# Performance work log

Measured on AMD Instinct MI355X. Metric: run time of the kernel, lower is better.

## Reference

```python
import jax, jax.numpy as jnp
import numpy as np

B, S, HID = 2, 1024, 2048
H, HK, D = 32, 4, 128
G = H // HK
EPS = 1e-6
SCALE = 1.0 / np.sqrt(D)
ROPE_THETA = 1000000.0


def _rope_tables(seq_len, dim, theta):
    inv_freq = 1.0 / (theta ** (np.arange(0, dim, 2, dtype=np.float32) / dim))
    t = np.arange(seq_len, dtype=np.float32)
    freqs = np.outer(t, inv_freq)                      # [S, D/2]
    emb = np.concatenate([freqs, freqs], axis=-1)       # [S, D]
    return (jnp.asarray(np.cos(emb))[None, :, None, :],
            jnp.asarray(np.sin(emb))[None, :, None, :])  # [1,S,1,D]


def setup_inputs() -> dict:
    key = jax.random.key(0)
    k1, k2, k3 = jax.random.split(key, 3)
    cos, sin = _rope_tables(S, D, ROPE_THETA)
    return {
        "hidden_states": jax.random.normal(k1, (B, S, HID), jnp.float32),
        "cos": cos,
        "sin": sin,
        "w_qkv": jax.random.normal(k2, (HID, (H + 2 * HK) * D), jnp.float32) * 0.02,
        "q_norm_w": jnp.ones((D,), jnp.float32),
        "k_norm_w": jnp.ones((D,), jnp.float32),
        "w_o": jax.random.normal(k3, (H * D, HID), jnp.float32) * 0.02,
    }


def _rms_norm(x, w):
    xf = x.astype(jnp.float32)
    var = jnp.mean(xf * xf, axis=-1, keepdims=True)
    return (w * (xf * jax.lax.rsqrt(var + EPS))).astype(x.dtype)


def _rotate_half(x):
    x1, x2 = jnp.split(x, 2, axis=-1)
    return jnp.concatenate([-x2, x1], axis=-1)


def reference(hidden_states, cos, sin, w_qkv, q_norm_w, k_norm_w, w_o):
    b, s, _ = hidden_states.shape
    qkv = hidden_states @ w_qkv                          # [B,S,(H+2HK)*D]
    q, k, v = jnp.split(qkv, [H * D, (H + HK) * D], axis=-1)
    q = q.reshape(b, s, H, D)
    k = k.reshape(b, s, HK, D)
    v = v.reshape(b, s, HK, D)
    # per-head RMSNorm on q/k, then rotary (BSH layout)
    q = _rms_norm(q, q_norm_w)
    k = _rms_norm(k, k_norm_w)
    q = q * cos + _rotate_half(q) * sin
    k = k * cos + _rotate_half(k) * sin
    # grouped-query causal SDPA (prefill path, sparse_mode=2)
    qg = q.reshape(b, s, HK, G, D)
    scores = jnp.einsum("bqkgd,bskd->bkgqs", qg, k) * SCALE  # [B,HK,G,S,S]
    causal = jnp.tril(jnp.ones((s, s), bool))
    scores = jnp.where(causal, scores, jnp.finfo(scores.dtype).min)
    probs = jax.nn.softmax(scores, axis=-1)
    ctx = jnp.einsum("bkgqs,bskd->bqkgd", probs, v)          # [B,S,HK,G,D]
    ctx = ctx.reshape(b, s, H * D)
    return ctx @ w_o                                          # [B,S,HID]
```

## Files before the change

### kernel.cpp

```cpp
#include <hip/hip_runtime.h>

#define B_   2
#define S_   1024
#define HID_ 2048
#define H_   32
#define HK_  4
#define D_   128
#define NQKV ((H_ + 2 * HK_) * D_)
#define TOK  (B_ * S_)

typedef short bf16x8  __attribute__((ext_vector_type(8)));
typedef short short4v __attribute__((ext_vector_type(4)));
typedef float f32x4   __attribute__((ext_vector_type(4)));
typedef int   i32x4   __attribute__((ext_vector_type(4)));

__device__ inline short f2bf(float f) {
  unsigned u = __builtin_bit_cast(unsigned, f);
  u += 0x7fffu + ((u >> 16) & 1u);
  return (short)(u >> 16);
}
__device__ inline float bf2f(short s) {
  return __builtin_bit_cast(float, ((unsigned)(unsigned short)s) << 16);
}

__device__ __forceinline__ void gld_lds16(const short* g, short* l) {
  __builtin_amdgcn_global_load_lds((__attribute__((address_space(1))) void*)g,
                                   (__attribute__((address_space(3))) void*)l, 16, 0, 0);
}

__global__ __launch_bounds__(256) void cast_f32_bf16(const float* __restrict__ in,
                                                     short* __restrict__ out, int n4) {
  int i = blockIdx.x * 256 + threadIdx.x;
  if (i >= n4) return;
  f32x4 v = ((const f32x4*)in)[i];
  short4v o;
  o[0] = f2bf(v[0]); o[1] = f2bf(v[1]); o[2] = f2bf(v[2]); o[3] = f2bf(v[3]);
  ((short4v*)out)[i] = o;
}

__global__ __launch_bounds__(256) void transpose_cast(const float* __restrict__ in,
                                                      short* __restrict__ out,
                                                      int K, int N) {
  __shared__ float tile[32][33];
  int nb = blockIdx.x * 32, kb = blockIdx.y * 32;
  int c = threadIdx.x & 31, r0 = threadIdx.x >> 5;
#pragma unroll
  for (int i = 0; i < 4; i++) {
    int r = r0 + i * 8;
    tile[r][c] = in[(size_t)(kb + r) * N + nb + c];
  }
  __syncthreads();
#pragma unroll
  for (int i = 0; i < 4; i++) {
    int r = r0 + i * 8;
    out[(size_t)(nb + r) * K + kb + c] = f2bf(tile[c][r]);
  }
}

__global__ __launch_bounds__(256) void gemm_bt128(const short* __restrict__ A,
                                                  const short* __restrict__ Bt,
                                                  float* __restrict__ C,
                                                  int M, int N, int Kfull, int klen) {
  const int tid  = threadIdx.x;
  const int m0   = blockIdx.y * 128;
  const int n0   = blockIdx.x * 128;
  const int kz0  = blockIdx.z * klen;
  const int w    = tid >> 6, lane = tid & 63;
  const int quad = lane >> 4, l16 = lane & 15;
  const int wm   = (w >> 1) * 64, wn = (w & 1) * 64;

  __shared__ short As[128 * 64];
  __shared__ short Bs[128 * 64];

  const f32x4 z = {0.f, 0.f, 0.f, 0.f};
  f32x4 acc[4][4];
#pragma unroll
  for (int i = 0; i < 4; i++)
#pragma unroll
    for (int j = 0; j < 4; j++) acc[i][j] = z;

  const int srow = lane >> 3;
  const int lc   = (lane & 7) ^ srow;

  for (int kk = 0; kk < klen; kk += 64) {
    const int k0 = kz0 + kk;
#pragma unroll
    for (int i = 0; i < 4; i++) {
      int rb = w * 32 + i * 8;
      gld_lds16(&A [(size_t)(m0 + rb + srow) * Kfull + k0 + lc * 8], &As[rb * 64]);
      gld_lds16(&Bt[(size_t)(n0 + rb + srow) * Kfull + k0 + lc * 8], &Bs[rb * 64]);
    }
    __syncthreads();
#pragma unroll
    for (int kb = 0; kb < 2; kb++) {
      const int pc = ((kb * 4 + quad) ^ (l16 & 7)) * 8;
      bf16x8 a[4], b[4];
#pragma unroll
      for (int f = 0; f < 4; f++) {
        a[f] = *(const bf16x8*)&As[(wm + f * 16 + l16) * 64 + pc];
        b[f] = *(const bf16x8*)&Bs[(wn + f * 16 + l16) * 64 + pc];
      }
#pragma unroll
      for (int fi = 0; fi < 4; fi++)
#pragma unroll
        for (int fj = 0; fj < 4; fj++)
          acc[fi][fj] = __builtin_amdgcn_mfma_f32_16x16x32_bf16(a[fi], b[fj], acc[fi][fj], 0, 0, 0);
    }
    __syncthreads();
  }

  float* Cz = C + (size_t)blockIdx.z * M * N;
#pragma unroll
  for (int fi = 0; fi < 4; fi++) {
    int row0 = m0 + wm + fi * 16 + quad * 4;
#pragma unroll
    for (int fj = 0; fj < 4; fj++) {
      int col = n0 + wn + fj * 16 + l16;
#pragma unroll
      for (int r = 0; r < 4; r++)
        Cz[(size_t)(row0 + r) * N + col] = acc[fi][fj][r];
    }
  }
}

__global__ __launch_bounds__(256) void add2(const float* __restrict__ a,
                                            const float* __restrict__ b,
                                            float* __restrict__ c, int n4) {
  int i = blockIdx.x * 256 + threadIdx.x;
  if (i >= n4) return;
  f32x4 va = ((const f32x4*)a)[i], vb = ((const f32x4*)b)[i];
  ((f32x4*)c)[i] = va + vb;
}

__global__ __launch_bounds__(256) void gemm_qkv(const short* __restrict__ A,
                                                const short* __restrict__ Bt,
                                                const float* __restrict__ cosT,
                                                const float* __restrict__ sinT,
                                                const float* __restrict__ qw,
                                                const float* __restrict__ kw,
                                                short* __restrict__ Qb,
                                                short* __restrict__ Kb,
                                                short* __restrict__ Vt) {
  const int tid  = threadIdx.x;
  const int m0   = blockIdx.y * 128;
  const int n0   = blockIdx.x * 128;
  const int w    = tid >> 6, lane = tid & 63;
  const int quad = lane >> 4, l16 = lane & 15;
  const int wm   = (w >> 1) * 64, wn = (w & 1) * 64;

  __shared__ short As[128 * 64];
  __shared__ short Bs[128 * 64];
  __shared__ float ss_lds[4][64];

  const f32x4 z = {0.f, 0.f, 0.f, 0.f};
  f32x4 acc[4][4];
#pragma unroll
  for (int i = 0; i < 4; i++)
#pragma unroll
    for (int j = 0; j < 4; j++) acc[i][j] = z;

  const int srow = lane >> 3;
  const int lc   = (lane & 7) ^ srow;

  for (int k0 = 0; k0 < HID_; k0 += 64) {
#pragma unroll
    for (int i = 0; i < 4; i++) {
      int rb = w * 32 + i * 8;
      gld_lds16(&A [(size_t)(m0 + rb + srow) * HID_ + k0 + lc * 8], &As[rb * 64]);
      gld_lds16(&Bt[(size_t)(n0 + rb + srow) * HID_ + k0 + lc * 8], &Bs[rb * 64]);
    }
    __syncthreads();
#pragma unroll
    for (int kb = 0; kb < 2; kb++) {
      const int pc = ((kb * 4 + quad) ^ (l16 & 7)) * 8;
      bf16x8 a[4], b[4];
#pragma unroll
      for (int f = 0; f < 4; f++) {
        a[f] = *(const bf16x8*)&As[(wm + f * 16 + l16) * 64 + pc];
        b[f] = *(const bf16x8*)&Bs[(wn + f * 16 + l16) * 64 + pc];
      }
#pragma unroll
      for (int fi = 0; fi < 4; fi++)
#pragma unroll
        for (int fj = 0; fj < 4; fj++)
          acc[fi][fj] = __builtin_amdgcn_mfma_f32_16x16x32_bf16(a[fi], b[fj], acc[fi][fj], 0, 0, 0);
    }
    __syncthreads();
  }

  const int hd = n0 >> 7;
  const int bb = m0 >> 10;
  const int sW = (m0 & (S_ - 1)) + wm;

  if (hd >= H_ + HK_) {
    const int khv = hd - (H_ + HK_);
    short* dstV = Vt + ((size_t)(bb * HK_ + khv) * D_) * S_;
#pragma unroll
    for (int fi = 0; fi < 4; fi++) {
      int s = sW + fi * 16 + quad * 4;
#pragma unroll
      for (int fj = 0; fj < 4; fj++) {
        int d = wn + fj * 16 + l16;
        short4v o;
#pragma unroll
        for (int r = 0; r < 4; r++) o[r] = f2bf(acc[fi][fj][r]);
        *(short4v*)&dstV[(size_t)d * S_ + s] = o;
      }
    }
    return;
  }

  float ssp[4][4];
#pragma unroll
  for (int fi = 0; fi < 4; fi++)
#pragma unroll
    for (int r = 0; r < 4; r++) {
      float t = 0.f;
#pragma unroll
      for (int fj = 0; fj < 4; fj++) t += acc[fi][fj][r] * acc[fi][fj][r];
      ssp[fi][r] = t;
    }
#pragma unroll
  for (int off = 1; off < 16; off <<= 1)
#pragma unroll
    for (int fi = 0; fi < 4; fi++)
#pragma unroll
      for (int r = 0; r < 4; r++) ssp[fi][r] += __shfl_xor(ssp[fi][r], off, 64);
  if (l16 == 0)
#pragma unroll
    for (int fi = 0; fi < 4; fi++)
#pragma unroll
      for (int r = 0; r < 4; r++) ss_lds[w][fi * 16 + quad * 4 + r] = ssp[fi][r];
  __syncthreads();
  float rn[4][4];
#pragma unroll
  for (int fi = 0; fi < 4; fi++)
#pragma unroll
    for (int r = 0; r < 4; r++) {
      int row = fi * 16 + quad * 4 + r;
      rn[fi][r] = rsqrtf((ss_lds[w][row] + ss_lds[w ^ 1][row]) * (1.0f / 128.0f) + 1e-6f);
    }
  const float* wv = (hd < H_) ? qw : kw;
  float wgt[4];
#pragma unroll
  for (int fj = 0; fj < 4; fj++) wgt[fj] = wv[wn + fj * 16 + l16];

  short* xown = (w & 1) ? &Bs[(w >> 1) * 4096] : &As[(w >> 1) * 4096];
  short* xpar = (w & 1) ? &As[(w >> 1) * 4096] : &Bs[(w >> 1) * 4096];
#pragma unroll
  for (int fi = 0; fi < 4; fi++)
#pragma unroll
    for (int fj = 0; fj < 4; fj++) {
      short4v y4;
#pragma unroll
      for (int r = 0; r < 4; r++) y4[r] = f2bf(acc[fi][fj][r] * rn[fi][r] * wgt[fj]);
      *(short4v*)&xown[(((fi * 4 + fj) * 4 + quad) * 16 + l16) * 4] = y4;
    }
  __syncthreads();

  const float sign = (wn == 0) ? -1.0f : 1.0f;
  const float osc  = (hd < H_) ? (0.08838834764831845f * 1.4426950408889634f) : 1.0f;
  short* dstQ = (hd < H_) ? (Qb + (((size_t)bb * H_ + hd) * S_) * D_)
                          : (Kb + (((size_t)bb * HK_ + (hd - H_)) * S_) * D_);
#pragma unroll
  for (int fi = 0; fi < 4; fi++)
#pragma unroll
    for (int fj = 0; fj < 4; fj++) {
      short4v yp4 = *(const short4v*)&xpar[(((fi * 4 + fj) * 4 + quad) * 16 + l16) * 4];
      int d = wn + fj * 16 + l16;
#pragma unroll
      for (int r = 0; r < 4; r++) {
        int s = sW + fi * 16 + quad * 4 + r;
        float y  = acc[fi][fj][r] * rn[fi][r] * wgt[fj];
        float yp = bf2f(yp4[r]);
        float c  = cosT[s * D_ + d];
        float sn = sinT[s * D_ + d];
        dstQ[(size_t)s * D_ + d] = f2bf((y * c + sign * yp * sn) * osc);
      }
    }
}

__global__ __launch_bounds__(256) void attn_mfma5(const short* __restrict__ Qb,
                                                  const short* __restrict__ Kb,
                                                  const short* __restrict__ Vt,
                                                  short* __restrict__ ctx) {
  const int qmap[8] = {7, 0, 6, 1, 5, 2, 4, 3};
  const int qt = qmap[blockIdx.x & 7];
  const int h  = blockIdx.y;
  const int b  = blockIdx.z;
  const int kh = h >> 3;
  const int q0 = qt * 128;
  const int tid = threadIdx.x, w = tid >> 6, lane = tid & 63;
  const int quad = lane >> 4, l16 = lane & 15;
  const float MBIAS = 18.0f;

  __shared__ short Ks[128 * 64];
  __shared__ short Vs[144 * 64];
  __shared__ short Ps[4][2][16 * 72];

  for (int i = tid; i < 16 * 64; i += 256) Vs[128 * 64 + i] = (short)0x3F80;

  const short* Qbase = Qb + (((size_t)b * H_ + h) * S_ + q0) * D_;
  bf16x8 aq[2][4];
#pragma unroll
  for (int fi = 0; fi < 2; fi++)
#pragma unroll
    for (int kb = 0; kb < 4; kb++)
      aq[fi][kb] = *(const bf16x8*)&Qbase[(size_t)(fi * 64 + w * 16 + l16) * D_ + kb * 32 + quad * 8];

  const f32x4 z = {0.f, 0.f, 0.f, 0.f};
  f32x4 O[2][9];
#pragma unroll
  for (int fi = 0; fi < 2; fi++)
#pragma unroll
    for (int n = 0; n < 9; n++) O[fi][n] = z;

  const short* Kbase = Kb + ((size_t)(b * HK_ + kh) * S_) * D_;
  const short* Vbase = Vt + ((size_t)(b * HK_ + kh) * D_) * S_;

  const int srow = lane >> 3;
  const int lc   = (lane & 7) ^ srow;

  const int nkt = 2 * qt + 2;
  for (int kt = 0; kt < nkt; kt++) {
    const int k0 = kt * 64;
    __syncthreads();
#pragma unroll
    for (int i = 0; i < 4; i++) {
      int rb = w * 32 + i * 8;
      int rr = rb + srow;
      gld_lds16(&Kbase[(size_t)(k0 + (rr & 63)) * D_ + (rr >> 6) * 64 + lc * 8], &Ks[rb * 64]);
      gld_lds16(&Vbase[(size_t)rr * S_ + k0 + lc * 8], &Vs[rb * 64]);
    }
    __syncthreads();

#pragma unroll
    for (int nb = 0; nb < 4; nb++) {
      f32x4 s0 = z, s1 = z;
#pragma unroll
      for (int kb = 0; kb < 4; kb++) {
        const int c  = kb * 4 + quad;
        const int c7 = c & 7;
        const int rr = (c >> 3) * 64 + nb * 16 + l16;
        bf16x8 bk = *(const bf16x8*)&Ks[rr * 64 + (c7 ^ (l16 & 7)) * 8];
        s0 = __builtin_amdgcn_mfma_f32_16x16x32_bf16(aq[0][kb], bk, s0, 0, 0, 0);
        s1 = __builtin_amdgcn_mfma_f32_16x16x32_bf16(aq[1][kb], bk, s1, 0, 0, 0);
      }
      const int col = k0 + nb * 16 + l16;
#pragma unroll
      for (int r = 0; r < 4; r++) {
        int row0 = q0 + w * 16 + quad * 4 + r;
        float p0 = (col > row0) ? 0.0f : exp2f(s0[r] - MBIAS);
        float p1 = (col > row0 + 64) ? 0.0f : exp2f(s1[r] - MBIAS);
        Ps[w][0][(quad * 4 + r) * 72 + nb * 16 + l16] = f2bf(p0);
        Ps[w][1][(quad * 4 + r) * 72 + nb * 16 + l16] = f2bf(p1);
      }
    }

#pragma unroll
    for (int kb2 = 0; kb2 < 2; kb2++) {
      bf16x8 ap0 = *(const bf16x8*)&Ps[w][0][l16 * 72 + kb2 * 32 + quad * 8];
      bf16x8 ap1 = *(const bf16x8*)&Ps[w][1][l16 * 72 + kb2 * 32 + quad * 8];
      const int c7 = kb2 * 4 + quad;
#pragma unroll
      for (int nb2 = 0; nb2 < 9; nb2++) {
        int d = nb2 * 16 + l16;
        bf16x8 bv = *(const bf16x8*)&Vs[d * 64 + (c7 ^ (d & 7)) * 8];
        O[0][nb2] = __builtin_amdgcn_mfma_f32_16x16x32_bf16(ap0, bv, O[0][nb2], 0, 0, 0);
        O[1][nb2] = __builtin_amdgcn_mfma_f32_16x16x32_bf16(ap1, bv, O[1][nb2], 0, 0, 0);
      }
    }
  }

#pragma unroll
  for (int fi = 0; fi < 2; fi++)
#pragma unroll
    for (int r = 0; r < 4; r++) {
      float inv = 1.0f / O[fi][8][r];
      size_t row = (size_t)(b * S_ + q0 + fi * 64 + w * 16 + quad * 4 + r);
      short* dst = ctx + row * (H_ * D_) + h * D_;
#pragma unroll
      for (int nb2 = 0; nb2 < 8; nb2++)
        dst[nb2 * 16 + l16] = f2bf(O[fi][nb2][r] * inv);
    }
}

extern "C" void kernel_launch(void* const* d_in, const int* in_sizes, int n_in,
                              void* d_out, int out_size, void* d_ws, size_t ws_size,
                              hipStream_t stream) {
  (void)in_sizes; (void)n_in; (void)out_size; (void)ws_size;
  const float* hidden = (const float*)d_in[0];
  const float* cosT   = (const float*)d_in[1];
  const float* sinT   = (const float*)d_in[2];
  const float* wqkv   = (const float*)d_in[3];
  const float* qnw    = (const float*)d_in[4];
  const float* knw    = (const float*)d_in[5];
  const float* wo     = (const float*)d_in[6];
  float* out = (float*)d_out;

  char* ws = (char*)d_ws;
  short* Qb  = (short*)ws;
  short* Kb  = (short*)(ws + 16777216);
  short* Vt  = (short*)(ws + 16777216 + 2097152);
  short* hb  = (short*)(ws + 41943040);
  short* wT  = (short*)(ws + 41943040 + 8388608);
  short* ctx = (short*)(ws + 41943040 + 8388608 + 20971520);
  float* part = (float*)ws;

  cast_f32_bf16<<<4096, 256, 0, stream>>>(hidden, hb, TOK * HID_ / 4);
  transpose_cast<<<dim3(NQKV / 32, HID_ / 32), 256, 0, stream>>>(wqkv, wT, HID_, NQKV);
  gemm_qkv<<<dim3(NQKV / 128, TOK / 128), 256, 0, stream>>>(hb, wT, cosT, sinT, qnw, knw, Qb, Kb, Vt);
  attn_mfma5<<<dim3(S_ / 128, H_, B_), 256, 0, stream>>>(Qb, Kb, Vt, ctx);
  transpose_cast<<<dim3(HID_ / 32, (H_ * D_) / 32), 256, 0, stream>>>(wo, wT, H_ * D_, HID_);
  gemm_bt128<<<dim3(HID_ / 128, TOK / 128, 2), 256, 0, stream>>>(ctx, wT, part, TOK, HID_, H_ * D_, (H_ * D_) / 2);
  add2<<<(TOK * HID_ / 4 + 255) / 256, 256, 0, stream>>>(part, part + (size_t)TOK * HID_, out, TOK * HID_ / 4);
}
```

Before: 330.9 us.

## Transpose QKV GEMM tile for Q/K heads so RoPE pairs stay in-register

For Q/K head tiles the GEMM swaps operand roles so each thread's accumulator holds head-dim elements along rows. Fragments are assigned so the rotate-half partners (d and d+64) land in the same thread. This removes the LDS round-trip and extra barrier used to exchange partner values, and lets the cos/sin loads, weight loads and output stores be vectorized. The RMS reduction also needs fewer shuffles. The V path keeps the old orientation, at the cost of more complex per-tile indexing and different LDS read patterns.

```diff
diff --git a/kernel.cpp b/kernel.cpp
--- a/kernel.cpp
+++ b/kernel.cpp
@@ -146,11 +146,13 @@
   const int n0   = blockIdx.x * 128;
   const int w    = tid >> 6, lane = tid & 63;
   const int quad = lane >> 4, l16 = lane & 15;
-  const int wm   = (w >> 1) * 64, wn = (w & 1) * 64;
+
+  const int hd   = n0 >> 7;
+  const bool isv = (hd >= H_ + HK_);
 
   __shared__ short As[128 * 64];
   __shared__ short Bs[128 * 64];
-  __shared__ float ss_lds[4][64];
+  __shared__ float ss_lds[2][128];
 
   const f32x4 z = {0.f, 0.f, 0.f, 0.f};
   f32x4 acc[4][4];
@@ -161,6 +163,15 @@
 
   const int srow = lane >> 3;
   const int lc   = (lane & 7) ^ srow;
+
+  const short* srcA = isv ? As : Bs;
+  const short* srcB = isv ? Bs : As;
+  int rA[4], rB[4];
+#pragma unroll
+  for (int f = 0; f < 4; f++) {
+    rA[f] = isv ? ((w >> 1) * 64 + f * 16) : ((w >> 1) * 16 + f * 32);
+    rB[f] = (w & 1) * 64 + f * 16;
+  }
 
   for (int k0 = 0; k0 < HID_; k0 += 64) {
 #pragma unroll
@@ -176,8 +187,8 @@
       bf16x8 a[4], b[4];
 #pragma unroll
       for (int f = 0; f < 4; f++) {
-        a[f] = *(const bf16x8*)&As[(wm + f * 16 + l16) * 64 + pc];
-        b[f] = *(const bf16x8*)&Bs[(wn + f * 16 + l16) * 64 + pc];
+        a[f] = *(const bf16x8*)&srcA[(rA[f] + l16) * 64 + pc];
+        b[f] = *(const bf16x8*)&srcB[(rB[f] + l16) * 64 + pc];
       }
 #pragma unroll
       for (int fi = 0; fi < 4; fi++)
@@ -188,19 +199,18 @@
     __syncthreads();
   }
 
-  const int hd = n0 >> 7;
   const int bb = m0 >> 10;
-  const int sW = (m0 & (S_ - 1)) + wm;
-
-  if (hd >= H_ + HK_) {
+  const int s0 = m0 & (S_ - 1);
+
+  if (isv) {
     const int khv = hd - (H_ + HK_);
     short* dstV = Vt + ((size_t)(bb * HK_ + khv) * D_) * S_;
 #pragma unroll
     for (int fi = 0; fi < 4; fi++) {
-      int s = sW + fi * 16 + quad * 4;
+      int s = s0 + (w >> 1) * 64 + fi * 16 + quad * 4;
 #pragma unroll
       for (int fj = 0; fj < 4; fj++) {
-        int d = wn + fj * 16 + l16;
+        int d = (w & 1) * 64 + fj * 16 + l16;
         short4v o;
 #pragma unroll
         for (int r = 0; r < 4; r++) o[r] = f2bf(acc[fi][fj][r]);
@@ -210,74 +220,67 @@
     return;
   }
 
-  float ssp[4][4];
+  const int dqbase = (w >> 1) * 16 + quad * 4;
+
+  float ssp[4];
+#pragma unroll
+  for (int fj = 0; fj < 4; fj++) {
+    float t = 0.f;
+#pragma unroll
+    for (int fi = 0; fi < 4; fi++)
+#pragma unroll
+      for (int r = 0; r < 4; r++) t += acc[fi][fj][r] * acc[fi][fj][r];
+    ssp[fj] = t;
+  }
+#pragma unroll
+  for (int fj = 0; fj < 4; fj++) {
+    ssp[fj] += __shfl_xor(ssp[fj], 16, 64);
+    ssp[fj] += __shfl_xor(ssp[fj], 32, 64);
+  }
+  if (quad == 0)
+#pragma unroll
+    for (int fj = 0; fj < 4; fj++)
+      ss_lds[w >> 1][(w & 1) * 64 + fj * 16 + l16] = ssp[fj];
+  __syncthreads();
+  float rn[4];
+#pragma unroll
+  for (int fj = 0; fj < 4; fj++) {
+    int t = (w & 1) * 64 + fj * 16 + l16;
+    rn[fj] = rsqrtf((ss_lds[0][t] + ss_lds[1][t]) * (1.0f / 128.0f) + 1e-6f);
+  }
+
+  const float* wv = (hd < H_) ? qw : kw;
+  f32x4 wgt[4];
 #pragma unroll
   for (int fi = 0; fi < 4; fi++)
-#pragma unroll
-    for (int r = 0; r < 4; r++) {
-      float t = 0.f;
-#pragma unroll
-      for (int fj = 0; fj < 4; fj++) t += acc[fi][fj][r] * acc[fi][fj][r];
-      ssp[fi][r] = t;
-    }
-#pragma unroll
-  for (int off = 1; off < 16; off <<= 1)
-#pragma unroll
-    for (int fi = 0; fi < 4; fi++)
-#pragma unroll
-      for (int r = 0; r < 4; r++) ssp[fi][r] += __shfl_xor(ssp[fi][r], off, 64);
-  if (l16 == 0)
-#pragma unroll
-    for (int fi = 0; fi < 4; fi++)
-#pragma unroll
-      for (int r = 0; r < 4; r++) ss_lds[w][fi * 16 + quad * 4 + r] = ssp[fi][r];
-  __syncthreads();
-  float rn[4][4];
-#pragma unroll
-  for (int fi = 0; fi < 4; fi++)
-#pragma unroll
-    for (int r = 0; r < 4; r++) {
-      int row = fi * 16 + quad * 4 + r;
-      rn[fi][r] = rsqrtf((ss_lds[w][row] + ss_lds[w ^ 1][row]) * (1.0f / 128.0f) + 1e-6f);
-    }
-  const float* wv = (hd < H_) ? qw : kw;
-  float wgt[4];
-#pragma unroll
-  for (int fj = 0; fj < 4; fj++) wgt[fj] = wv[wn + fj * 16 + l16];
-
-  short* xown = (w & 1) ? &Bs[(w >> 1) * 4096] : &As[(w >> 1) * 4096];
-  short* xpar = (w & 1) ? &As[(w >> 1) * 4096] : &Bs[(w >> 1) * 4096];
-#pragma unroll
-  for (int fi = 0; fi < 4; fi++)
-#pragma unroll
-    for (int fj = 0; fj < 4; fj++) {
-      short4v y4;
-#pragma unroll
-      for (int r = 0; r < 4; r++) y4[r] = f2bf(acc[fi][fj][r] * rn[fi][r] * wgt[fj]);
-      *(short4v*)&xown[(((fi * 4 + fj) * 4 + quad) * 16 + l16) * 4] = y4;
-    }
-  __syncthreads();
-
-  const float sign = (wn == 0) ? -1.0f : 1.0f;
-  const float osc  = (hd < H_) ? (0.08838834764831845f * 1.4426950408889634f) : 1.0f;
+    wgt[fi] = *(const f32x4*)&wv[dqbase + fi * 32];
+
+  const float osc = (hd < H_) ? (0.08838834764831845f * 1.4426950408889634f) : 1.0f;
   short* dstQ = (hd < H_) ? (Qb + (((size_t)bb * H_ + hd) * S_) * D_)
                           : (Kb + (((size_t)bb * HK_ + (hd - H_)) * S_) * D_);
-#pragma unroll
-  for (int fi = 0; fi < 4; fi++)
+
+#pragma unroll
+  for (int f2 = 0; f2 < 2; f2++) {
+    const int dlo = dqbase + f2 * 32;
 #pragma unroll
     for (int fj = 0; fj < 4; fj++) {
-      short4v yp4 = *(const short4v*)&xpar[(((fi * 4 + fj) * 4 + quad) * 16 + l16) * 4];
-      int d = wn + fj * 16 + l16;
+      const int s = s0 + (w & 1) * 64 + fj * 16 + l16;
+      f32x4 cl = *(const f32x4*)&cosT[(size_t)s * D_ + dlo];
+      f32x4 sl = *(const f32x4*)&sinT[(size_t)s * D_ + dlo];
+      f32x4 ch = *(const f32x4*)&cosT[(size_t)s * D_ + dlo + 64];
+      f32x4 sh = *(const f32x4*)&sinT[(size_t)s * D_ + dlo + 64];
+      short4v olo, ohi;
 #pragma unroll
       for (int r = 0; r < 4; r++) {
-        int s = sW + fi * 16 + quad * 4 + r;
-        float y  = acc[fi][fj][r] * rn[fi][r] * wgt[fj];
-        float yp = bf2f(yp4[r]);
-        float c  = cosT[s * D_ + d];
-        float sn = sinT[s * D_ + d];
-        dstQ[(size_t)s * D_ + d] = f2bf((y * c + sign * yp * sn) * osc);
-      }
-    }
+        float y1 = acc[f2][fj][r]     * wgt[f2][r]     * rn[fj];
+        float y2 = acc[f2 + 2][fj][r] * wgt[f2 + 2][r] * rn[fj];
+        olo[r] = f2bf((y1 * cl[r] - y2 * sl[r]) * osc);
+        ohi[r] = f2bf((y2 * ch[r] + y1 * sh[r]) * osc);
+      }
+      *(short4v*)&dstQ[(size_t)s * D_ + dlo]      = olo;
+      *(short4v*)&dstQ[(size_t)s * D_ + dlo + 64] = ohi;
+    }
+  }
 }
 
 __global__ __launch_bounds__(256) void attn_mfma5(const short* __restrict__ Qb,
```

Result: no change. 334.2 us (+1.0%).
